# Kernel optimization log

Measured on AMD Instinct MI355X. Metric: run time of the kernel, lower is better.

The kernel has to match this reference:

```python
import jax, jax.numpy as jnp
import numpy as np
import math

B, S, HID = 2, 4096, 2048
H, D, C = 16, 128, 256  # heads, head_dim, chunk (block) size
NC = S // C


def _build_slopes(n):
    # faithful port of MiniMaxText01LinearAttention._build_slope_tensor
    def p2(m):
        start = 2.0 ** (-(2.0 ** (-(math.log2(m) - 3))))
        return [start * (start ** i) for i in range(m)]
    if math.log2(n).is_integer():
        sl = p2(n)
    else:
        cp = 2 ** math.floor(math.log2(n))
        sl = p2(cp) + p2(2 * cp)[0::2][: n - cp]
    return np.asarray(sl, dtype=np.float32).reshape(n, 1, 1)


def setup_inputs() -> dict:
    key = jax.random.key(0)
    k1, k2, k3, k4 = jax.random.split(key, 4)
    x = jax.random.normal(k1, (B, S, HID), dtype=jnp.float32)
    w_qkv = jax.random.normal(k2, (HID, 3 * H * D), dtype=jnp.float32) * 0.02
    w_gate = jax.random.normal(k3, (HID, H * D), dtype=jnp.float32) * 0.02
    w_out = jax.random.normal(k4, (H * D, HID), dtype=jnp.float32) * 0.02
    slopes = jnp.asarray(_build_slopes(H))  # [H,1,1]
    return {"x": x, "w_qkv": w_qkv, "w_gate": w_gate, "w_out": w_out, "slopes": slopes}


def _to_chunks(t):
    # [B,S,H*D] -> [NC,B,H,C,D]
    return (t.reshape(B, S, H, D)
             .transpose(0, 2, 1, 3)          # [B,H,S,D]
             .reshape(B, H, NC, C, D)
             .transpose(2, 0, 1, 3, 4))      # [NC,B,H,C,D]


def _lightning_attn(q, k, v, slopes):
    # q,k,v: [NC,B,H,C,D]; slopes: [H,1,1]
    s = slopes
    pos = jnp.arange(C, dtype=jnp.float32)
    q_decay = jnp.exp(-s * (pos + 1.0).reshape(1, C, 1))        # [H,C,1]
    k_decay = jnp.exp(-s * (C - 1.0 - pos).reshape(1, C, 1))    # [H,C,1]
    idx = pos[:, None] - pos[None, :]                            # [C,C]
    diag_decay = jnp.where(idx >= 0, jnp.exp(-s * idx), 0.0)     # [H,C,C]
    block_decay = jnp.exp(-s * float(C))[None]                   # [1,H,1,1]

    def step(kv, qkv_c):
        qc, kc, vc = qkv_c  # each [B,H,C,D]
        # intra-chunk (causal, decayed)
        scores = jnp.einsum('bhid,bhjd->bhij', qc, kc) * diag_decay
        o = jnp.einsum('bhij,bhjd->bhid', scores, vc)
        # inter-chunk via recurrent state kv: [B,H,D,D]
        o = o + jnp.einsum('bhid,bhde->bhie', qc * q_decay, kv)
        kv = block_decay * kv + jnp.einsum('bhjd,bhje->bhde', kc * k_decay, vc)
        return kv, o

    kv0 = jnp.zeros((B, H, D, D), dtype=q.dtype)
    _, outs = jax.lax.scan(step, kv0, (q, k, v))  # outs: [NC,B,H,C,D]
    return (outs.transpose(1, 2, 0, 3, 4)          # [B,H,NC,C,D]
                .reshape(B, H, S, D)
                .transpose(0, 2, 1, 3)
                .reshape(B, S, H * D))


def reference(x, w_qkv, w_gate, w_out, slopes):
    qkv = jax.nn.silu(x @ w_qkv)                   # act on fused qkv (hidden_act=silu)
    q, k, v = jnp.split(qkv, 3, axis=-1)
    attn = _lightning_attn(_to_chunks(q), _to_chunks(k), _to_chunks(v), slopes)
    gate = jax.nn.sigmoid(x @ w_gate)              # output gate
    return (gate * attn) @ w_out
```

## Files before the change

kernel.cpp:

```cpp
#include <hip/hip_runtime.h>

typedef __bf16 bf16;
typedef __bf16 bf16x8 __attribute__((ext_vector_type(8)));
typedef __bf16 bf16x4 __attribute__((ext_vector_type(4)));
typedef float  f32x4  __attribute__((ext_vector_type(4)));

#define B_   2
#define S_   4096
#define HID_ 2048
#define H_   16
#define D_   128
#define C_   256
#define NC_  16
#define M_   (B_*S_)
#define K_   2048

typedef __attribute__((address_space(1))) const void gas_t;
typedef __attribute__((address_space(3))) void las_t;

__global__ void cvt_kernel(const float* __restrict__ x,
                           const float* __restrict__ wqkv,
                           const float* __restrict__ wgate,
                           const float* __restrict__ wout,
                           bf16* __restrict__ xb, bf16* __restrict__ wT) {
    __shared__ float tile[32][33];
    int bid = blockIdx.x, tid = threadIdx.x;
    if (bid < 8192) {
        int idx = (bid * 256 + tid) * 8;
        float4 f0 = *(const float4*)(x + idx);
        float4 f1 = *(const float4*)(x + idx + 4);
        bf16x8 o;
        o[0] = (bf16)f0.x; o[1] = (bf16)f0.y; o[2] = (bf16)f0.z; o[3] = (bf16)f0.w;
        o[4] = (bf16)f1.x; o[5] = (bf16)f1.y; o[6] = (bf16)f1.z; o[7] = (bf16)f1.w;
        *(bf16x8*)(xb + idx) = o;
        return;
    }
    bid -= 8192;
    int k0 = (bid & 63) * 32, n0 = (bid >> 6) * 32;
    const float* src; int ld, col0;
    if (n0 < 6144)      { src = wqkv;  ld = 6144; col0 = n0; }
    else if (n0 < 8192) { src = wgate; ld = 2048; col0 = n0 - 6144; }
    else                { src = wout;  ld = 2048; col0 = n0 - 8192; }
    int tx = tid & 31, ty = tid >> 5;
#pragma unroll
    for (int i = 0; i < 4; i++) {
        int kk = ty + i * 8;
        tile[kk][tx] = src[(size_t)(k0 + kk) * ld + col0 + tx];
    }
    __syncthreads();
#pragma unroll
    for (int i = 0; i < 4; i++) {
        int nn = ty + i * 8;
        wT[(size_t)(n0 + nn) * K_ + k0 + tx] = (bf16)tile[tx][nn];
    }
}

#define DSRA(dst, buf, tb) do {                                              \
    const bf16* _p = SMEM + ((buf) * 2 + wr) * 8192;                         \
    _Pragma("unroll")                                                        \
    for (int _t = 0; _t < 4; _t++) {                                         \
        const int _r = ((tb) + _t) * 16 + l15;                               \
        dst[_t][0] = *(const bf16x8*)(_p + _r * 64 + ps0);                   \
        dst[_t][1] = *(const bf16x8*)(_p + _r * 64 + ps1);                   \
    }                                                                        \
} while (0)

#define DSRB(dst, buf, tb) do {                                              \
    const bf16* _p = SMEM + 32768 + ((buf) * 2 + wch) * 8192;                \
    _Pragma("unroll")                                                        \
    for (int _t = 0; _t < 2; _t++) {                                         \
        const int _r = bro + ((tb) + _t) * 16 + l15;                         \
        dst[_t][0] = *(const bf16x8*)(_p + _r * 64 + ps0);                   \
        dst[_t][1] = *(const bf16x8*)(_p + _r * 64 + ps1);                   \
    }                                                                        \
} while (0)

#define STAGE_A(buf, h, kt) do {                                             \
    const bf16* _s = Ag + (size_t)(h) * (128 * K_) + (kt) * 64;              \
    bf16* _d = SMEM + ((buf) * 2 + (h)) * 8192 + srow * 64 + sslot * 8;      \
    __builtin_amdgcn_global_load_lds((gas_t*)_s, (las_t*)_d, 16, 0, 0);      \
    __builtin_amdgcn_global_load_lds((gas_t*)(_s + (size_t)64 * K_),         \
                                     (las_t*)(_d + 4096), 16, 0, 0);         \
} while (0)

#define STAGE_B(buf, h, kt) do {                                             \
    const bf16* _s = Bg + (size_t)(h) * (128 * K_) + (kt) * 64;              \
    bf16* _d = SMEM + 32768 + ((buf) * 2 + (h)) * 8192 + srow * 64 + sslot * 8; \
    __builtin_amdgcn_global_load_lds((gas_t*)_s, (las_t*)_d, 16, 0, 0);      \
    __builtin_amdgcn_global_load_lds((gas_t*)(_s + (size_t)64 * K_),         \
                                     (las_t*)(_d + 4096), 16, 0, 0);         \
} while (0)

#define MM8(afr, bfr, ib, jb) do {                                           \
    _Pragma("unroll")                                                        \
    for (int _i = 0; _i < 4; _i++)                                           \
        _Pragma("unroll")                                                    \
        for (int _j = 0; _j < 2; _j++)                                       \
            _Pragma("unroll")                                                \
            for (int _k = 0; _k < 2; _k++)                                   \
                acc[(ib) + _i][(jb) + _j] =                                  \
                    __builtin_amdgcn_mfma_f32_16x16x32_bf16(                 \
                        afr[_i][_k], bfr[_j][_k],                            \
                        acc[(ib) + _i][(jb) + _j], 0, 0, 0);                 \
} while (0)

#define PTAIL(...) do {                                                      \
    __builtin_amdgcn_s_barrier();                                            \
    asm volatile("s_waitcnt lgkmcnt(0)" ::: "memory");                       \
    __builtin_amdgcn_s_setprio(1);                                           \
    __VA_ARGS__;                                                             \
    __builtin_amdgcn_s_setprio(0);                                           \
    __builtin_amdgcn_s_barrier();                                            \
} while (0)

#define VMC6 asm volatile("s_waitcnt vmcnt(6)" ::: "memory")
#define VMC0 asm volatile("s_waitcnt vmcnt(0)" ::: "memory")

template <int MODE>
__global__ __launch_bounds__(512, 2) void gemm_kernel(
        const bf16* __restrict__ A, const bf16* __restrict__ Bm,
        bf16* __restrict__ qo, bf16* __restrict__ ko,
        bf16* __restrict__ go, bf16* __restrict__ vTd,
        bf16* __restrict__ kTd, const float* __restrict__ slopes,
        float* __restrict__ out) {
    __shared__ __align__(16) bf16 SMEM[65536];
    const int m0 = blockIdx.x * 256, n0 = blockIdx.y * 256;
    const int tid = threadIdx.x, lane = tid & 63, wid = tid >> 6;
    const int quad = lane >> 4, l15 = lane & 15;
    const int wr = wid >> 2, wc = wid & 3;
    const int wch = wc >> 1, bro = (wc & 1) * 64;
    const int srow = tid >> 3, sslot = tid & 7;
    const int lcol = (sslot ^ (srow & 7)) * 8;
    const int ps0 = ((quad)     ^ (l15 & 7)) * 8;
    const int ps1 = ((quad + 4) ^ (l15 & 7)) * 8;
    const bf16* Ag = A  + (size_t)(m0 + srow) * K_ + lcol;
    const bf16* Bg = Bm + (size_t)(n0 + srow) * K_ + lcol;

    f32x4 acc[8][4] = {};
    bf16x8 aLo[4][2], aHi[4][2], bLo[2][2], bHi[2][2];

    STAGE_A(0, 0, 0); STAGE_A(0, 1, 0);
    STAGE_B(0, 0, 0); STAGE_B(0, 1, 0);
    STAGE_B(1, 0, 1); STAGE_B(1, 1, 1);
    STAGE_A(1, 0, 1);
    VMC6;
    __builtin_amdgcn_s_barrier();

#pragma unroll 1
    for (int it = 0; it < 16; ++it) {
        const bool last = (it == 15);
        const int t2 = 2 * it + 2, t3 = 2 * it + 3;
        DSRA(aLo, 0, 0); DSRB(bLo, 0, 0);
        STAGE_A(1, 1, 2 * it + 1);
        PTAIL(MM8(aLo, bLo, 0, 0));
        DSRB(bHi, 0, 2);
        PTAIL(MM8(aLo, bHi, 0, 2));
        DSRA(aHi, 0, 4);
        if (!last) { STAGE_B(0, 0, t2); STAGE_B(0, 1, t2); }
        PTAIL(MM8(aHi, bLo, 4, 0));
        if (!last) STAGE_A(0, 0, t2);
        if (last) VMC0; else VMC6;
        PTAIL(MM8(aHi, bHi, 4, 2));
        DSRA(aLo, 1, 0); DSRB(bLo, 1, 0);
        if (!last) STAGE_A(0, 1, t2);
        PTAIL(MM8(aLo, bLo, 0, 0));
        DSRB(bHi, 1, 2);
        PTAIL(MM8(aLo, bHi, 0, 2));
        DSRA(aHi, 1, 4);
        if (!last) { STAGE_B(1, 0, t3); STAGE_B(1, 1, t3); }
        PTAIL(MM8(aHi, bLo, 4, 0));
        if (!last) STAGE_A(1, 0, t3);
        if (last) VMC0; else VMC6;
        PTAIL(MM8(aHi, bHi, 4, 2));
    }

    const int rb = m0 + wr * 128;
    if (MODE == 0) {
        const int kind = n0 >> 11;
        const int cb = n0 & 2047;
        if (kind != 2) {
            bf16* outb = (kind == 0) ? qo : (kind == 1) ? ko : go;
            const bool silu = (kind < 3);
#pragma unroll
            for (int ti = 0; ti < 8; ti++)
#pragma unroll
                for (int tj = 0; tj < 4; tj++)
#pragma unroll
                    for (int r = 0; r < 4; r++) {
                        int row = rb + ti * 16 + quad * 4 + r;
                        int col = cb + wc * 64 + tj * 16 + l15;
                        float xv = acc[ti][tj][r];
                        float sg = 1.f / (1.f + __expf(-xv));
                        float av = silu ? xv * sg : sg;
                        outb[(size_t)row * 2048 + col] = (bf16)av;
                    }
        }
        if (kind == 1 || kind == 2) {
#pragma unroll
            for (int ti = 0; ti < 8; ti++)
#pragma unroll
                for (int tj = 0; tj < 4; tj++) {
                    int c = wc * 64 + tj * 16 + l15;
                    int s0 = wr * 128 + ti * 16 + quad * 4;
                    bf16x4 t4;
#pragma unroll
                    for (int r = 0; r < 4; r++) {
                        float xv = acc[ti][tj][r];
                        float sg = 1.f / (1.f + __expf(-xv));
                        t4[r] = (bf16)(xv * sg);
                    }
                    int byt = (c * 512 + s0 * 2) ^ ((c & 7) << 4);
                    *(bf16x4*)((char*)SMEM + byt) = t4;
                }
            __syncthreads();
            bf16* dstT = (kind == 2) ? vTd : kTd;
            const int bq = m0 >> 12, sbase = m0 & 4095, hb = cb >> 7;
            const int l = tid & 31, rg = tid >> 5;
#pragma unroll 1
            for (int p = 0; p < 16; ++p) {
                int c = p * 16 + rg;
                int byt = (c * 512 + l * 16) ^ ((c & 7) << 4);
                bf16x8 vv = *(const bf16x8*)((const char*)SMEM + byt);
                int h = hb + (c >> 7), d = c & 127;
                if (kind == 1) {
                    float sl = slopes[h];
                    float e = __expf(-sl * (float)(255 - l * 8));
                    float rr = __expf(sl);
#pragma unroll
                    for (int i = 0; i < 8; i++) {
                        vv[i] = (bf16)((float)vv[i] * e);
                        e *= rr;
                    }
                }
                *(bf16x8*)(dstT + ((size_t)(bq * 16 + h) * 128 + d) * (size_t)S_
                           + sbase + l * 8) = vv;
            }
        }
    } else {
#pragma unroll
        for (int ti = 0; ti < 8; ti++)
#pragma unroll
            for (int tj = 0; tj < 4; tj++)
#pragma unroll
                for (int r = 0; r < 4; r++) {
                    int row = rb + ti * 16 + quad * 4 + r;
                    int col = n0 + wc * 64 + tj * 16 + l15;
                    out[(size_t)row * 2048 + col] = acc[ti][tj][r];
                }
    }
}

#undef DSRA
#undef DSRB
#undef STAGE_A
#undef STAGE_B
#undef MM8
#undef PTAIL
#undef VMC6
#undef VMC0

__global__ __launch_bounds__(256) void pass_a_kernel(
        const bf16* __restrict__ kT, const bf16* __restrict__ vT,
        bf16* __restrict__ KVT) {
    int c = blockIdx.x, bh = blockIdx.y;
    int tid = threadIdx.x, lane = tid & 63, wid = tid >> 6;
    int quad = lane >> 4, l15 = lane & 15;
    int e0 = (wid >> 1) * 64, d0 = (wid & 1) * 64;
    const bf16* vb = vT + (size_t)bh * 128 * S_ + c * 256;
    const bf16* kb = kT + (size_t)bh * 128 * S_ + c * 256;
    f32x4 acc[4][4] = {};
    for (int kbs = 0; kbs < 256; kbs += 32) {
        int j0 = kbs + quad * 8;
        bf16x8 af[4], bfr[4];
#pragma unroll
        for (int t = 0; t < 4; t++)
            af[t] = *(const bf16x8*)(vb + (size_t)(e0 + t * 16 + l15) * S_ + j0);
#pragma unroll
        for (int t = 0; t < 4; t++)
            bfr[t] = *(const bf16x8*)(kb + (size_t)(d0 + t * 16 + l15) * S_ + j0);
#pragma unroll
        for (int ti = 0; ti < 4; ti++)
#pragma unroll
            for (int tj = 0; tj < 4; tj++)
                acc[ti][tj] = __builtin_amdgcn_mfma_f32_16x16x32_bf16(
                    af[ti], bfr[tj], acc[ti][tj], 0, 0, 0);
    }
    size_t base = ((size_t)c * 32 + bh) * 16384;
#pragma unroll
    for (int ti = 0; ti < 4; ti++)
#pragma unroll
        for (int tj = 0; tj < 4; tj++)
#pragma unroll
            for (int r = 0; r < 4; r++) {
                int e = e0 + ti * 16 + quad * 4 + r, d = d0 + tj * 16 + l15;
                KVT[base + (size_t)e * 128 + d] = (bf16)acc[ti][tj][r];
            }
}

__global__ void scan_kernel(const bf16* __restrict__ KVT,
                            const float* __restrict__ slopes,
                            bf16* __restrict__ stT) {
    int slice = blockIdx.x, bh = blockIdx.y;
    float s = slopes[bh & 15];
    float bd = __expf(-s * 256.f);
    size_t off = (size_t)slice * 1024 + threadIdx.x * 4;
    float kv0 = 0.f, kv1 = 0.f, kv2 = 0.f, kv3 = 0.f;
    for (int c = 0; c < 16; c++) {
        size_t idx = ((size_t)c * 32 + bh) * 16384 + off;
        bf16x4 st;
        st[0] = (bf16)kv0; st[1] = (bf16)kv1; st[2] = (bf16)kv2; st[3] = (bf16)kv3;
        *(bf16x4*)(stT + idx) = st;
        bf16x4 kvc = *(const bf16x4*)(KVT + idx);
        kv0 = bd * kv0 + (float)kvc[0];
        kv1 = bd * kv1 + (float)kvc[1];
        kv2 = bd * kv2 + (float)kvc[2];
        kv3 = bd * kv3 + (float)kvc[3];
    }
}

__global__ __launch_bounds__(256) void pass_c_kernel(
        const bf16* __restrict__ q, const bf16* __restrict__ kk,
        const bf16* __restrict__ vT, const bf16* __restrict__ stT,
        const bf16* __restrict__ gate, const float* __restrict__ slopes,
        bf16* __restrict__ og) {
    __shared__ __align__(16) bf16 P[256 * 72];
    __shared__ float dtab[257];
    int c = blockIdx.x, bh = blockIdx.y, b = bh >> 4, h = bh & 15;
    int tid = threadIdx.x, lane = tid & 63, wid = tid >> 6;
    int quad = lane >> 4, l15 = lane & 15;
    int i0 = wid * 64;
    float s = slopes[h];
    dtab[tid] = __expf(-s * (float)tid);
    if (tid == 0) dtab[256] = __expf(-s * 256.f);
    __syncthreads();
    const bf16* qb = q  + ((size_t)(b * S_ + c * 256)) * 2048 + h * 128;
    const bf16* kb = kk + ((size_t)(b * S_ + c * 256)) * 2048 + h * 128;
    const bf16* vb = vT + (size_t)bh * 128 * S_ + c * 256;
    const bf16* st = stT + ((size_t)c * 32 + bh) * 16384;
    f32x4 acc[4][8] = {};

    for (int kbs = 0; kbs < 128; kbs += 32) {
        bf16x8 af[4];
#pragma unroll
        for (int t = 0; t < 4; t++)
            af[t] = *(const bf16x8*)(qb + (size_t)(i0 + t * 16 + l15) * 2048 + kbs + quad * 8);
#pragma unroll
        for (int te = 0; te < 8; te++) {
            bf16x8 bfr = *(const bf16x8*)(st + (size_t)(te * 16 + l15) * 128 + kbs + quad * 8);
#pragma unroll
            for (int t = 0; t < 4; t++)
                acc[t][te] = __builtin_amdgcn_mfma_f32_16x16x32_bf16(
                    af[t], bfr, acc[t][te], 0, 0, 0);
        }
    }
#pragma unroll
    for (int t = 0; t < 4; t++) {
        float qd[4];
#pragma unroll
        for (int r = 0; r < 4; r++) qd[r] = dtab[i0 + t * 16 + quad * 4 + r + 1];
#pragma unroll
        for (int te = 0; te < 8; te++)
#pragma unroll
            for (int r = 0; r < 4; r++) acc[t][te][r] *= qd[r];
    }

    for (int jt = 0; jt <= wid; jt++) {
        f32x4 sacc[4][4] = {};
        for (int kbs = 0; kbs < 128; kbs += 32) {
            bf16x8 af[4], bkr[4];
#pragma unroll
            for (int t = 0; t < 4; t++)
                af[t] = *(const bf16x8*)(qb + (size_t)(i0 + t * 16 + l15) * 2048 + kbs + quad * 8);
#pragma unroll
            for (int t = 0; t < 4; t++)
                bkr[t] = *(const bf16x8*)(kb + (size_t)(jt * 64 + t * 16 + l15) * 2048 + kbs + quad * 8);
#pragma unroll
            for (int ti = 0; ti < 4; ti++)
#pragma unroll
                for (int tj = 0; tj < 4; tj++)
                    sacc[ti][tj] = __builtin_amdgcn_mfma_f32_16x16x32_bf16(
                        af[ti], bkr[tj], sacc[ti][tj], 0, 0, 0);
        }
#pragma unroll
        for (int ti = 0; ti < 4; ti++)
#pragma unroll
            for (int tj = 0; tj < 4; tj++)
#pragma unroll
                for (int r = 0; r < 4; r++) {
                    int i = i0 + ti * 16 + quad * 4 + r;
                    int j = jt * 64 + tj * 16 + l15;
                    int diff = i - j;
                    float pv = (diff >= 0) ? sacc[ti][tj][r] * dtab[diff] : 0.f;
                    P[i * 72 + tj * 16 + l15] = (bf16)pv;
                }
#pragma unroll
        for (int k2 = 0; k2 < 64; k2 += 32) {
            bf16x8 af[4];
#pragma unroll
            for (int t = 0; t < 4; t++)
                af[t] = *(const bf16x8*)&P[(i0 + t * 16 + l15) * 72 + k2 + quad * 8];
#pragma unroll
            for (int te = 0; te < 8; te++) {
                bf16x8 bfr = *(const bf16x8*)(vb + (size_t)(te * 16 + l15) * S_ + jt * 64 + k2 + quad * 8);
#pragma unroll
                for (int t = 0; t < 4; t++)
                    acc[t][te] = __builtin_amdgcn_mfma_f32_16x16x32_bf16(
                        af[t], bfr, acc[t][te], 0, 0, 0);
            }
        }
    }

    const bf16* gb = gate + ((size_t)(b * S_ + c * 256)) * 2048 + h * 128;
    bf16* ob = og + ((size_t)(b * S_ + c * 256)) * 2048 + h * 128;
#pragma unroll
    for (int ti = 0; ti < 4; ti++)
#pragma unroll
        for (int te = 0; te < 8; te++)
#pragma unroll
            for (int r = 0; r < 4; r++) {
                int i = i0 + ti * 16 + quad * 4 + r;
                int e = te * 16 + l15;
                float gv = (float)gb[(size_t)i * 2048 + e];
                ob[(size_t)i * 2048 + e] = (bf16)(acc[ti][te][r] * gv);
            }
}

extern "C" void kernel_launch(void* const* d_in, const int* in_sizes, int n_in,
                              void* d_out, int out_size, void* d_ws, size_t ws_size,
                              hipStream_t stream) {
    const float* x      = (const float*)d_in[0];
    const float* wqkv   = (const float*)d_in[1];
    const float* wgate  = (const float*)d_in[2];
    const float* wout   = (const float*)d_in[3];
    const float* slopes = (const float*)d_in[4];
    float* out = (float*)d_out;

    bf16* wT   = (bf16*)d_ws;
    bf16* xb   = wT   + (size_t)10240 * 2048;
    bf16* qb   = xb   + (size_t)8192 * 2048;
    bf16* kbuf = qb   + (size_t)8192 * 2048;
    bf16* kTn  = kbuf + (size_t)8192 * 2048;
    bf16* gbuf = kTn  + (size_t)8192 * 2048;
    bf16* ogb  = kTn;
    bf16* vT   = (bf16*)d_out;
    bf16* KVT  = vT + (size_t)32 * 128 * 4096;
    bf16* stT  = KVT + (size_t)16 * 32 * 16384;

    cvt_kernel<<<dim3(28672), dim3(256), 0, stream>>>(x, wqkv, wgate, wout, xb, wT);
    gemm_kernel<0><<<dim3(32, 32), dim3(512), 0, stream>>>(
        xb, wT, qb, kbuf, gbuf, vT, kTn, slopes, (float*)nullptr);
    pass_a_kernel<<<dim3(16, 32), dim3(256), 0, stream>>>(kTn, vT, KVT);
    scan_kernel<<<dim3(16, 32), dim3(256), 0, stream>>>(KVT, slopes, stT);
    pass_c_kernel<<<dim3(16, 32), dim3(256), 0, stream>>>(
        qb, kbuf, vT, stT, gbuf, slopes, ogb);
    gemm_kernel<1><<<dim3(32, 8), dim3(512), 0, stream>>>(
        ogb, wT + (size_t)8192 * 2048, nullptr, nullptr, nullptr, nullptr,
        nullptr, nullptr, out);
}
```

Measured before the change: 606.8 us.

## Software-pipeline LDS fragment reads one phase ahead of MFMA blocks in GEMM

Restructures the GEMM main loop so the LDS reads for the next MFMA phase are issued right after the barrier, before the current phase's MFMAs. It also drops the explicit lgkmcnt(0) wait, so LDS latency can overlap with matrix math. The first fragment reads move before the loop, and each iteration's last phase prefetches the next iteration's fragments. The cost is more live fragment registers. Correctness now depends on the compiler inserting the right lgkmcnt waits, and on each read being ordered after the barrier that protects the staged LDS data.

```diff
diff --git a/kernel.cpp b/kernel.cpp
--- a/kernel.cpp
+++ b/kernel.cpp
@@ -104,12 +104,14 @@
                         acc[(ib) + _i][(jb) + _j], 0, 0, 0);                 \
 } while (0)
 
-#define PTAIL(...) do {                                                      \
+#define PH(RD, MMA) do {                                                     \
     __builtin_amdgcn_s_barrier();                                            \
-    asm volatile("s_waitcnt lgkmcnt(0)" ::: "memory");                       \
+    asm volatile("" ::: "memory");                                           \
+    RD;                                                                      \
     __builtin_amdgcn_s_setprio(1);                                           \
-    __VA_ARGS__;                                                             \
+    MMA;                                                                     \
     __builtin_amdgcn_s_setprio(0);                                           \
+    asm volatile("" ::: "memory");                                           \
     __builtin_amdgcn_s_barrier();                                            \
 } while (0)
 
@@ -145,33 +147,29 @@
     STAGE_A(1, 0, 1);
     VMC6;
     __builtin_amdgcn_s_barrier();
+    DSRA(aLo, 0, 0); DSRB(bLo, 0, 0);
 
 #pragma unroll 1
     for (int it = 0; it < 16; ++it) {
         const bool last = (it == 15);
         const int t2 = 2 * it + 2, t3 = 2 * it + 3;
-        DSRA(aLo, 0, 0); DSRB(bLo, 0, 0);
         STAGE_A(1, 1, 2 * it + 1);
-        PTAIL(MM8(aLo, bLo, 0, 0));
-        DSRB(bHi, 0, 2);
-        PTAIL(MM8(aLo, bHi, 0, 2));
-        DSRA(aHi, 0, 4);
+        PH(DSRB(bHi, 0, 2), MM8(aLo, bLo, 0, 0));
+        PH(DSRA(aHi, 0, 4), MM8(aLo, bHi, 0, 2));
         if (!last) { STAGE_B(0, 0, t2); STAGE_B(0, 1, t2); }
-        PTAIL(MM8(aHi, bLo, 4, 0));
+        PH((void)0, MM8(aHi, bLo, 4, 0));
         if (!last) STAGE_A(0, 0, t2);
         if (last) VMC0; else VMC6;
-        PTAIL(MM8(aHi, bHi, 4, 2));
-        DSRA(aLo, 1, 0); DSRB(bLo, 1, 0);
+        PH(DSRA(aLo, 1, 0); DSRB(bLo, 1, 0), MM8(aHi, bHi, 4, 2));
         if (!last) STAGE_A(0, 1, t2);
-        PTAIL(MM8(aLo, bLo, 0, 0));
-        DSRB(bHi, 1, 2);
-        PTAIL(MM8(aLo, bHi, 0, 2));
-        DSRA(aHi, 1, 4);
+        PH(DSRB(bHi, 1, 2), MM8(aLo, bLo, 0, 0));
+        PH(DSRA(aHi, 1, 4), MM8(aLo, bHi, 0, 2));
         if (!last) { STAGE_B(1, 0, t3); STAGE_B(1, 1, t3); }
-        PTAIL(MM8(aHi, bLo, 4, 0));
+        PH((void)0, MM8(aHi, bLo, 4, 0));
         if (!last) STAGE_A(1, 0, t3);
         if (last) VMC0; else VMC6;
-        PTAIL(MM8(aHi, bHi, 4, 2));
+        if (last) { PH((void)0, MM8(aHi, bHi, 4, 2)); }
+        else      { PH(DSRA(aLo, 0, 0); DSRB(bLo, 0, 0), MM8(aHi, bHi, 4, 2)); }
     }
 
     const int rb = m0 + wr * 128;
@@ -255,7 +253,7 @@
 #undef STAGE_A
 #undef STAGE_B
 #undef MM8
-#undef PTAIL
+#undef PH
 #undef VMC6
 #undef VMC0
 
```

New measurement: 1.341 ms. +121.0%, slower.
